# Kernel tuning notes

Hardware: AMD Instinct MI355X
Metric: run time of the kernel (lower is better)

The kernel has to match this reference:

```python
import jax, jax.numpy as jnp
import numpy as np

NUM_CONCEPTS = 4096
CONCEPT_DIM = 512


def setup_inputs() -> dict:
    key = jax.random.key(0)
    k1, k2 = jax.random.split(key)
    inp = jax.random.normal(k1, (8, 4096, CONCEPT_DIM), dtype=jnp.float32)
    bound = 1.0 / NUM_CONCEPTS
    codebook = jax.random.uniform(
        k2, (NUM_CONCEPTS, CONCEPT_DIM), dtype=jnp.float32,
        minval=-bound, maxval=bound)
    return {"inp": inp, "codebook": codebook}


def reference(inp, codebook):
    # flatten tokens: [N, D]
    flat = inp.reshape(-1, inp.shape[-1])
    # squared Euclidean distances [N, K]; argmin is identical to cdist argmin
    d2 = (
        jnp.sum(flat * flat, axis=1, keepdims=True)
        - 2.0 * jnp.einsum("nd,kd->nk", flat, codebook)
        + jnp.sum(codebook * codebook, axis=1)[None, :]
    )
    idx = jnp.argmin(d2, axis=1)  # [N]
    quantized = jnp.take(codebook, idx, axis=0).reshape(inp.shape)
    return quantized
```

## Files before the change

### kernel.cpp

```cpp
#include <hip/hip_runtime.h>
#include <math.h>

constexpr int D  = 512;
constexpr int K  = 4096;
constexpr int BM = 64;
constexpr int BN = 64;
constexpr int BD_LEG = 32;
constexpr int PAD = 4;

#define MARGIN 2.5e-3f
constexpr int RCAP = 12;
constexpr unsigned CAPQ = 4194304u;

typedef short short8v __attribute__((ext_vector_type(8)));
typedef float f32x4   __attribute__((ext_vector_type(4)));
typedef int   int4v   __attribute__((ext_vector_type(4)));

constexpr size_t SC_OFF   = 0;
constexpr size_t SX_OFF   = 16384;
constexpr size_t KEYS_OFF = 147456;
constexpr size_t QCNT_OFF = 409600;
constexpr size_t SCS_OFF  = 413696;
constexpr size_t SXS_OFF  = 430080;
constexpr size_t CBP_OFF  = 561152;
constexpr size_t WS_NEED  = CBP_OFF + (size_t)K * D;

__device__ inline unsigned ordkey(float f) {
    unsigned u = __float_as_uint(f);
    return (u & 0x80000000u) ? ~u : (u | 0x80000000u);
}
__device__ inline float fromkey(unsigned k) {
    unsigned u = (k & 0x80000000u) ? (k ^ 0x80000000u) : ~k;
    return __uint_as_float(u);
}
__device__ inline void gload16(const void* g, void* l) {
    __builtin_amdgcn_global_load_lds(
        (const __attribute__((address_space(1))) unsigned*)g,
        (__attribute__((address_space(3))) unsigned*)l, 16, 0, 0);
}

__global__ __launch_bounds__(256)
void prep_kernel(const float* __restrict__ cb, const float* __restrict__ inp,
                 float* __restrict__ sc, float* __restrict__ scs,
                 unsigned char* __restrict__ cbp,
                 float* __restrict__ sxg, float* __restrict__ sxs,
                 unsigned char* __restrict__ ap,
                 unsigned* __restrict__ qcnt, int nb_cb) {
    const int t = threadIdx.x;
    if (blockIdx.x == 0 && t == 0) *qcnt = 0u;
    const bool isCB = (int)blockIdx.x < nb_cb;
    const int r = t >> 2, p = t & 3;
    const int row = (isCB ? (int)blockIdx.x : ((int)blockIdx.x - nb_cb)) * 64 + r;
    const float* base = (isCB ? cb : inp) + (size_t)row * D + p * 128;

    float s = 0.0f, m = 0.0f;
#pragma unroll
    for (int g = 0; g < 16; ++g) {
        float4 v0 = *(const float4*)(base + g * 8);
        float4 v1 = *(const float4*)(base + g * 8 + 4);
        s = fmaf(v0.x, v0.x, s); s = fmaf(v0.y, v0.y, s);
        s = fmaf(v0.z, v0.z, s); s = fmaf(v0.w, v0.w, s);
        s = fmaf(v1.x, v1.x, s); s = fmaf(v1.y, v1.y, s);
        s = fmaf(v1.z, v1.z, s); s = fmaf(v1.w, v1.w, s);
        m = fmaxf(m, fmaxf(fmaxf(fabsf(v0.x), fabsf(v0.y)), fmaxf(fabsf(v0.z), fabsf(v0.w))));
        m = fmaxf(m, fmaxf(fmaxf(fabsf(v1.x), fabsf(v1.y)), fmaxf(fabsf(v1.z), fabsf(v1.w))));
    }
    s += __shfl_xor(s, 1, 64);
    s += __shfl_xor(s, 2, 64);
    m = fmaxf(m, __shfl_xor(m, 1, 64));
    m = fmaxf(m, __shfl_xor(m, 2, 64));
    const float sinv  = (m > 0.0f) ? 127.0f / m : 0.0f;
    const float scale = m * (1.0f / 127.0f);
    if (p == 0) {
        if (isCB) { sc[row] = s;  scs[row] = scale; }
        else      { sxg[row] = s; sxs[row] = scale; }
    }

    const int rstride = isCB ? 256 : 128;
    const int tile    = isCB ? (row >> 8) : (row >> 7);
    const int rit     = isCB ? (row & 255) : (row & 127);
    unsigned char* dst = isCB ? cbp : ap;
    const size_t tbase = (size_t)tile * (32 * rstride);
#pragma unroll
    for (int g = 0; g < 16; ++g) {
        float4 v0 = *(const float4*)(base + g * 8);
        float4 v1 = *(const float4*)(base + g * 8 + 4);
        float xs[8] = {v0.x, v0.y, v0.z, v0.w, v1.x, v1.y, v1.z, v1.w};
        unsigned u0 = 0, u1 = 0;
#pragma unroll
        for (int i = 0; i < 4; ++i) {
            int q = (int)rintf(xs[i] * sinv);
            q = q > 127 ? 127 : (q < -127 ? -127 : q);
            u0 |= ((unsigned)(q & 255)) << (8 * i);
        }
#pragma unroll
        for (int i = 4; i < 8; ++i) {
            int q = (int)rintf(xs[i] * sinv);
            q = q > 127 ? 127 : (q < -127 ? -127 : q);
            u1 |= ((unsigned)(q & 255)) << (8 * (i - 4));
        }
        const int db = 2 * p + (g >> 3);
        const int j  = ((16 * p + g) >> 1) & 3;
        const size_t slot = tbase + (size_t)db * (4 * rstride) + (size_t)j * rstride + rit;
        *(unsigned*)(dst + slot * 16 + (g & 1) * 8)     = u0;
        *(unsigned*)(dst + slot * 16 + (g & 1) * 8 + 4) = u1;
    }
}

__device__ float exact_dot512(const float* __restrict__ x, const float* __restrict__ c) {
    float s = 0.0f;
#pragma unroll 4
    for (int i = 0; i < 128; ++i) {
        const float4 xv = *(const float4*)(x + i * 4);
        const float4 cv = *(const float4*)(c + i * 4);
        s = fmaf(xv.x, cv.x, s); s = fmaf(xv.y, cv.y, s);
        s = fmaf(xv.z, cv.z, s); s = fmaf(xv.w, cv.w, s);
    }
    return s;
}

__global__ __launch_bounds__(512)
void score_kernel(const unsigned char* __restrict__ a_perm,
                  const unsigned char* __restrict__ b_perm,
                  const float* __restrict__ sc, const float* __restrict__ scs,
                  const float* __restrict__ sxs,
                  char* __restrict__ records) {
    __shared__ __align__(16) unsigned char lds[2 * 24576];
    __shared__ unsigned minsh[128];
    __shared__ unsigned cntsh[128];
    __shared__ unsigned short listsh[128][RCAP];

    const int t    = threadIdx.x;
    const int lane = t & 63;
    const int w    = t >> 6;
    const int wm   = w >> 2;
    const int wn   = w & 3;
    const int l15  = lane & 15;
    const int lk   = lane >> 4;
    const int bm   = blockIdx.x >> 4;
    const int bn   = blockIdx.x & 15;

    const unsigned char* gA = a_perm + (size_t)bm * 65536  + (size_t)t * 16;
    const unsigned char* gB = b_perm + (size_t)bn * 131072 + (size_t)t * 16;

    if (t < 128) { minsh[t] = 0xFFFFFFFFu; cntsh[t] = 0u; }

    int4v acc[4][4];
#pragma unroll
    for (int i = 0; i < 4; ++i)
#pragma unroll
        for (int j = 0; j < 4; ++j) acc[i][j] = int4v{0, 0, 0, 0};

    auto STAGE = [&](int db, int dbuf) {
        gload16(gA + (size_t)db * 8192,         &lds[dbuf + t * 16]);
        gload16(gB + (size_t)db * 16384,        &lds[dbuf + 8192 + t * 16]);
        gload16(gB + (size_t)db * 16384 + 8192, &lds[dbuf + 16384 + t * 16]);
    };

    STAGE(0, 0);
    __syncthreads();

    const unsigned char* lbA = &lds[lk * 2048 + l15 * 16];
    const unsigned char* lbB = &lds[8192 + lk * 4096 + l15 * 16];
    const int mbase = wm * 1024;
    const int nbase = wn * 1024;

    auto COMPUTE = [&](int cur) {
        int4v af[4], bf[4];
#pragma unroll
        for (int mt = 0; mt < 4; ++mt)
            af[mt] = *(const int4v*)(lbA + cur + mbase + mt * 256);
#pragma unroll
        for (int nt = 0; nt < 4; ++nt)
            bf[nt] = *(const int4v*)(lbB + cur + nbase + nt * 256);
#pragma unroll
        for (int mt = 0; mt < 4; ++mt)
#pragma unroll
            for (int nt = 0; nt < 4; ++nt)
                acc[mt][nt] = __builtin_amdgcn_mfma_i32_16x16x64_i8(af[mt], bf[nt], acc[mt][nt], 0, 0, 0);
    };

    int sdb = 1;
#pragma unroll 1
    for (int p = 0; p < 4; ++p) {
        STAGE(sdb, 24576); ++sdb;
        COMPUTE(0);
        __syncthreads();
        if (p < 3) { STAGE(sdb, 0); ++sdb; }
        COMPUTE(24576);
        __syncthreads();
    }

    float scvv[4], scsv[4];
#pragma unroll
    for (int nt = 0; nt < 4; ++nt) {
        const int code = bn * 256 + wn * 64 + nt * 16 + l15;
        scvv[nt] = sc[code];
        scsv[nt] = scs[code];
    }
    float sxsv[4][4];
#pragma unroll
    for (int mt = 0; mt < 4; ++mt)
#pragma unroll
        for (int rr = 0; rr < 4; ++rr)
            sxsv[mt][rr] = sxs[bm * 128 + wm * 64 + mt * 16 + lk * 4 + rr];

#pragma unroll
    for (int mt = 0; mt < 4; ++mt)
#pragma unroll
        for (int nt = 0; nt < 4; ++nt)
#pragma unroll
            for (int rr = 0; rr < 4; ++rr) {
                const float df = (float)acc[mt][nt][rr];
                const float vv = fmaf(-2.0f * sxsv[mt][rr] * scsv[nt], df, scvv[nt]);
                acc[mt][nt][rr] = __float_as_int(vv);
            }
#define VACC(mt, nt, rr) __int_as_float(acc[mt][nt][rr])

#pragma unroll
    for (int mt = 0; mt < 4; ++mt)
#pragma unroll
        for (int rr = 0; rr < 4; ++rr) {
            float m4 = fminf(fminf(VACC(mt, 0, rr), VACC(mt, 1, rr)),
                             fminf(VACC(mt, 2, rr), VACC(mt, 3, rr)));
            m4 = fminf(m4, __shfl_xor(m4, 1, 64));
            m4 = fminf(m4, __shfl_xor(m4, 2, 64));
            m4 = fminf(m4, __shfl_xor(m4, 4, 64));
            m4 = fminf(m4, __shfl_xor(m4, 8, 64));
            if (l15 == 0) {
                const int tok = wm * 64 + mt * 16 + lk * 4 + rr;
                atomicMin(&minsh[tok], ordkey(m4));
            }
        }
    __syncthreads();

#pragma unroll
    for (int mt = 0; mt < 4; ++mt)
#pragma unroll
        for (int rr = 0; rr < 4; ++rr) {
            const int tok = wm * 64 + mt * 16 + lk * 4 + rr;
            const float tmn = fromkey(minsh[tok]) + MARGIN;
#pragma unroll
            for (int nt = 0; nt < 4; ++nt) {
                if (VACC(mt, nt, rr) <= tmn) {
                    unsigned p = atomicAdd(&cntsh[tok], 1u);
                    if (p < RCAP)
                        listsh[tok][p] = (unsigned short)(bn * 256 + wn * 64 + nt * 16 + l15);
                }
            }
        }
    __syncthreads();
#undef VACC

    if (t < 128) {
        const unsigned* lw = (const unsigned*)&listsh[t][0];
        uint4 r0, r1;
        r0.x = __float_as_uint(fromkey(minsh[t]));
        r0.y = cntsh[t];
        r0.z = lw[0]; r0.w = lw[1];
        r1.x = lw[2]; r1.y = lw[3]; r1.z = lw[4]; r1.w = lw[5];
        char* rp = records + ((size_t)(bm * 128 + t) * 16 + bn) * 32;
        *(uint4*)rp = r0;
        *(uint4*)(rp + 16) = r1;
    }
}

__global__ __launch_bounds__(256)
void compact_kernel(const char* __restrict__ records,
                    unsigned long long* __restrict__ keysg,
                    unsigned* __restrict__ qcnt,
                    unsigned* __restrict__ queue) {
    const int token = blockIdx.x * 256 + threadIdx.x;
    keysg[token] = 0xFFFFFFFFFFFFFFFFull;

    const char* rbase = records + (size_t)token * 16 * 32;
    float mn = __builtin_huge_valf();
#pragma unroll
    for (int i = 0; i < 16; ++i)
        mn = fminf(mn, *(const float*)(rbase + (size_t)i * 32));
    const float thr = mn + MARGIN;

    unsigned my = 0;
#pragma unroll 1
    for (int i = 0; i < 16; ++i) {
        const char* rp = rbase + (size_t)i * 32;
        if (*(const float*)rp <= thr) {
            const unsigned cnt = *(const unsigned*)(rp + 4);
            my += (cnt <= RCAP) ? cnt : 256u;
        }
    }
    unsigned pos = atomicAdd(qcnt, my);
#pragma unroll 1
    for (int i = 0; i < 16; ++i) {
        const char* rp = rbase + (size_t)i * 32;
        if (*(const float*)rp <= thr) {
            const unsigned cnt = *(const unsigned*)(rp + 4);
            if (cnt <= RCAP) {
                const unsigned short* cs = (const unsigned short*)(rp + 8);
                for (unsigned j = 0; j < cnt; ++j) {
                    if (pos < CAPQ) queue[pos] = ((unsigned)token << 12) | cs[j];
                    ++pos;
                }
            } else {
                for (int c2 = 0; c2 < 256; ++c2) {
                    if (pos < CAPQ) queue[pos] = ((unsigned)token << 12) | (unsigned)(i * 256 + c2);
                    ++pos;
                }
            }
        }
    }
}

__global__ __launch_bounds__(256)
void exec_kernel(const float* __restrict__ inp, const float* __restrict__ cb,
                 const float* __restrict__ sc, const float* __restrict__ sxg,
                 const unsigned* __restrict__ qcnt, const unsigned* __restrict__ queue,
                 unsigned long long* __restrict__ keysg, int nblk64) {
    const unsigned raw = *qcnt;
    unsigned total = raw > CAPQ ? CAPQ : raw;
    const unsigned stride = gridDim.x * 256;
    for (unsigned i = blockIdx.x * 256 + threadIdx.x; i < total; i += stride) {
        const unsigned e = queue[i];
        const int token = e >> 12;
        const int code  = e & 4095;
        const float dot = exact_dot512(inp + (size_t)token * D, cb + (size_t)code * D);
        const float tmp = sxg[token] - 2.0f * dot;
        const float v   = tmp + sc[code];
        const unsigned long long key =
            ((unsigned long long)__float_as_uint(v) << 32) | (unsigned)code;
        atomicMin(&keysg[token], key);
    }
    if (raw > CAPQ && blockIdx.x < (unsigned)nblk64) {
        const int t = threadIdx.x;
        const int m0 = blockIdx.x * 64;
#pragma unroll 1
        for (int tok = 0; tok < 64; ++tok) {
            const int token = m0 + tok;
            const float sxv = sxg[token];
            const float* xrow = inp + (size_t)token * D;
            for (int code = t; code < K; code += 256) {
                const float dot = exact_dot512(xrow, cb + (size_t)code * D);
                const float tmp = sxv - 2.0f * dot;
                const float v   = tmp + sc[code];
                const unsigned long long key =
                    ((unsigned long long)__float_as_uint(v) << 32) | (unsigned)code;
                atomicMin(&keysg[token], key);
            }
        }
    }
}

__global__ __launch_bounds__(256)
void gather_kernel(const float* __restrict__ cb,
                   const unsigned long long* __restrict__ keysg,
                   float* __restrict__ out) {
    const int m0 = blockIdx.x * 64;
    __shared__ int bidx[64];
    if (threadIdx.x < 64) bidx[threadIdx.x] = (int)(keysg[m0 + threadIdx.x] & 0xFFFFFFFFull);
    __syncthreads();
    for (int q = threadIdx.x; q < 64 * (D / 4); q += 256) {
        const int r = q >> 7;
        const int c = (q & 127) * 4;
        *(float4*)(out + (size_t)(m0 + r) * D + c) = *(const float4*)(cb + (size_t)bidx[r] * D + c);
    }
}

__global__ __launch_bounds__(256)
void sc_kernel(const float* __restrict__ cb, float* __restrict__ sc) {
    const int row  = blockIdx.x * 4 + (threadIdx.x >> 6);
    const int lane = threadIdx.x & 63;
    const float* r = cb + (size_t)row * D + lane * 8;
    float4 v0 = *(const float4*)r;
    float4 v1 = *(const float4*)(r + 4);
    float s = v0.x * v0.x;
    s += v0.y * v0.y; s += v0.z * v0.z; s += v0.w * v0.w;
    s += v1.x * v1.x; s += v1.y * v1.y; s += v1.z * v1.z; s += v1.w * v1.w;
#pragma unroll
    for (int off = 1; off < 64; off <<= 1) s += __shfl_xor(s, off, 64);
    if (lane == 0) sc[row] = s;
}

__global__ __launch_bounds__(256)
void vq_kernel(const float* __restrict__ inp, const float* __restrict__ cb,
               const float* __restrict__ sc, float* __restrict__ out) {
    __shared__ __align__(16) float As[BD_LEG][BM + PAD];
    __shared__ __align__(16) float Bs[BD_LEG][BN + PAD];
    __shared__ float sxl[BM];
    __shared__ float scs_l[BN];
    __shared__ int   bidx[BM];

    const int t  = threadIdx.x;
    const int m0 = blockIdx.x * BM;
    const int tm = t >> 4;
    const int tn = t & 15;
    const float FINF = __builtin_huge_valf();

    {
        const int r = t >> 2, p = t & 3;
        const float* row = inp + (size_t)(m0 + r) * D + p * 128;
        float s = 0.0f;
#pragma unroll
        for (int i = 0; i < 32; ++i) {
            float4 v = *(const float4*)(row + i * 4);
            s = fmaf(v.x, v.x, s); s = fmaf(v.y, v.y, s);
            s = fmaf(v.z, v.z, s); s = fmaf(v.w, v.w, s);
        }
        s += __shfl_xor(s, 1, 64);
        s += __shfl_xor(s, 2, 64);
        if (p == 0) sxl[r] = s;
    }
    __syncthreads();

    float sxm[4];
#pragma unroll
    for (int i = 0; i < 4; ++i) sxm[i] = sxl[tm * 4 + i];

    float runv[4] = {FINF, FINF, FINF, FINF};
    int   runi[4] = {0, 0, 0, 0};
    const int dq = (t & 7) << 2;
    const int mr = t >> 3;

#pragma unroll 1
    for (int kb = 0; kb < K; kb += BN) {
        __syncthreads();
        if (t < BN) scs_l[t] = sc[kb + t];

        float accl[4][4];
#pragma unroll
        for (int i = 0; i < 4; ++i)
#pragma unroll
            for (int j = 0; j < 4; ++j) accl[i][j] = 0.0f;

#pragma unroll 1
        for (int db = 0; db < D; db += BD_LEG) {
            const float* ap = inp + (size_t)(m0 + mr) * D + db + dq;
            const float* bp = cb  + (size_t)(kb + mr) * D + db + dq;
            float4 av0 = *(const float4*)ap;
            float4 av1 = *(const float4*)(ap + (size_t)32 * D);
            float4 bv0 = *(const float4*)bp;
            float4 bv1 = *(const float4*)(bp + (size_t)32 * D);
            __syncthreads();
            As[dq + 0][mr] = av0.x; As[dq + 1][mr] = av0.y;
            As[dq + 2][mr] = av0.z; As[dq + 3][mr] = av0.w;
            As[dq + 0][mr + 32] = av1.x; As[dq + 1][mr + 32] = av1.y;
            As[dq + 2][mr + 32] = av1.z; As[dq + 3][mr + 32] = av1.w;
            Bs[dq + 0][mr] = bv0.x; Bs[dq + 1][mr] = bv0.y;
            Bs[dq + 2][mr] = bv0.z; Bs[dq + 3][mr] = bv0.w;
            Bs[dq + 0][mr + 32] = bv1.x; Bs[dq + 1][mr + 32] = bv1.y;
            Bs[dq + 2][mr + 32] = bv1.z; Bs[dq + 3][mr + 32] = bv1.w;
            __syncthreads();
#pragma unroll
            for (int d = 0; d < BD_LEG; ++d) {
                const float4 a = *(const float4*)(&As[d][tm * 4]);
                const float4 b = *(const float4*)(&Bs[d][tn * 4]);
                float af[4] = {a.x, a.y, a.z, a.w};
                float bf[4] = {b.x, b.y, b.z, b.w};
#pragma unroll
                for (int i = 0; i < 4; ++i)
#pragma unroll
                    for (int j = 0; j < 4; ++j)
                        accl[i][j] = fmaf(af[i], bf[j], accl[i][j]);
            }
        }
#pragma unroll
        for (int i = 0; i < 4; ++i) {
            float bv = FINF;
            int   bi = 0x7fffffff;
#pragma unroll
            for (int j = 0; j < 4; ++j) {
                const float p = accl[i][j];
                const float tmp = sxm[i] - 2.0f * p;
                const float v   = tmp + scs_l[tn * 4 + j];
                const int  idx  = kb + tn * 4 + j;
                if (v < bv) { bv = v; bi = idx; }
            }
#pragma unroll
            for (int off = 1; off < 16; off <<= 1) {
                const float ov = __shfl_xor(bv, off, 64);
                const int   oi = __shfl_xor(bi, off, 64);
                if (ov < bv || (ov == bv && oi < bi)) { bv = ov; bi = oi; }
            }
            if (bv < runv[i]) { runv[i] = bv; runi[i] = bi; }
        }
    }
    if (tn == 0) {
#pragma unroll
        for (int i = 0; i < 4; ++i) bidx[tm * 4 + i] = runi[i];
    }
    __syncthreads();
#pragma unroll 1
    for (int q = t; q < BM * (D / 4); q += 256) {
        const int r = q >> 7;
        const int c = (q & 127) * 4;
        const float4 v = *(const float4*)(cb + (size_t)bidx[r] * D + c);
        *(float4*)(out + (size_t)(m0 + r) * D + c) = v;
    }
}

extern "C" void kernel_launch(void* const* d_in, const int* in_sizes, int n_in,
                              void* d_out, int out_size, void* d_ws, size_t ws_size,
                              hipStream_t stream) {
    const float* inp = (const float*)d_in[0];
    const float* cb  = (const float*)d_in[1];
    float* out = (float*)d_out;
    float* sc  = (float*)d_ws;
    const int tokens = in_sizes[0] / D;

    const bool fast = (ws_size >= WS_NEED) && (tokens % 256 == 0) &&
                      (in_sizes[1] == K * D) &&
                      ((size_t)out_size * 4 >= (size_t)tokens * D + (size_t)tokens * 16 * 32);

    if (fast) {
        float* sxg = (float*)((char*)d_ws + SX_OFF);
        unsigned long long* keysg = (unsigned long long*)((char*)d_ws + KEYS_OFF);
        unsigned* qcnt = (unsigned*)((char*)d_ws + QCNT_OFF);
        float* scsg = (float*)((char*)d_ws + SCS_OFF);
        float* sxsg = (float*)((char*)d_ws + SXS_OFF);
        unsigned char* cbp = (unsigned char*)((char*)d_ws + CBP_OFF);
        unsigned char* ap  = (unsigned char*)d_out;
        char* records = (char*)d_out + (size_t)tokens * D;
        unsigned* queue = (unsigned*)d_out;

        const int nb_cb = K / 64;

        prep_kernel<<<nb_cb + tokens / 64, 256, 0, stream>>>(cb, inp, sc, scsg, cbp,
                                                             sxg, sxsg, ap, qcnt, nb_cb);
        score_kernel<<<(tokens / 128) * 16, 512, 0, stream>>>(ap, cbp, sc, scsg, sxsg, records);
        compact_kernel<<<tokens / 256, 256, 0, stream>>>(records, keysg, qcnt, queue);
        exec_kernel<<<2048, 256, 0, stream>>>(inp, cb, sc, sxg, qcnt, queue, keysg, tokens / 64);
        gather_kernel<<<tokens / 64, 256, 0, stream>>>(cb, keysg, out);
    } else {
        sc_kernel<<<K / 4, 256, 0, stream>>>(cb, sc);
        vq_kernel<<<tokens / BM, 256, 0, stream>>>(inp, cb, sc, out);
    }
}
```

Before: 286.9 us.

## Fuse compact, exec and gather into one per-block resolve kernel with LDS queue

Replaces the global candidate queue, global atomic counter and three separate kernels (compact, exact-rescore, gather) with a single resolve kernel in which each 64-token block builds its candidate list in shared memory, rescores candidates exactly with LDS atomicMin, and gathers the winning codebook rows. This removes two kernel launches, the global queue traffic and the global atomics. In exchange, parallelism is limited to tokens/64 blocks, so load imbalance between blocks is possible, and any block whose list overflows LCAP falls back to a full 4096-code brute-force scan done by that one block.

```diff
diff --git a/kernel.cpp b/kernel.cpp
--- a/kernel.cpp
+++ b/kernel.cpp
@@ -10,7 +10,7 @@
 
 #define MARGIN 2.5e-3f
 constexpr int RCAP = 12;
-constexpr unsigned CAPQ = 4194304u;
+constexpr int LCAP = 3072;
 
 typedef short short8v __attribute__((ext_vector_type(8)));
 typedef float f32x4   __attribute__((ext_vector_type(4)));
@@ -18,11 +18,9 @@
 
 constexpr size_t SC_OFF   = 0;
 constexpr size_t SX_OFF   = 16384;
-constexpr size_t KEYS_OFF = 147456;
-constexpr size_t QCNT_OFF = 409600;
-constexpr size_t SCS_OFF  = 413696;
-constexpr size_t SXS_OFF  = 430080;
-constexpr size_t CBP_OFF  = 561152;
+constexpr size_t SCS_OFF  = 147456;
+constexpr size_t SXS_OFF  = 163840;
+constexpr size_t CBP_OFF  = 294912;
 constexpr size_t WS_NEED  = CBP_OFF + (size_t)K * D;
 
 __device__ inline unsigned ordkey(float f) {
@@ -44,10 +42,8 @@
                  float* __restrict__ sc, float* __restrict__ scs,
                  unsigned char* __restrict__ cbp,
                  float* __restrict__ sxg, float* __restrict__ sxs,
-                 unsigned char* __restrict__ ap,
-                 unsigned* __restrict__ qcnt, int nb_cb) {
+                 unsigned char* __restrict__ ap, int nb_cb) {
     const int t = threadIdx.x;
-    if (blockIdx.x == 0 && t == 0) *qcnt = 0u;
     const bool isCB = (int)blockIdx.x < nb_cb;
     const int r = t >> 2, p = t & 3;
     const int row = (isCB ? (int)blockIdx.x : ((int)blockIdx.x - nb_cb)) * 64 + r;
@@ -266,99 +262,95 @@
 }
 
 __global__ __launch_bounds__(256)
-void compact_kernel(const char* __restrict__ records,
-                    unsigned long long* __restrict__ keysg,
-                    unsigned* __restrict__ qcnt,
-                    unsigned* __restrict__ queue) {
-    const int token = blockIdx.x * 256 + threadIdx.x;
-    keysg[token] = 0xFFFFFFFFFFFFFFFFull;
-
-    const char* rbase = records + (size_t)token * 16 * 32;
-    float mn = __builtin_huge_valf();
-#pragma unroll
-    for (int i = 0; i < 16; ++i)
-        mn = fminf(mn, *(const float*)(rbase + (size_t)i * 32));
-    const float thr = mn + MARGIN;
-
-    unsigned my = 0;
-#pragma unroll 1
-    for (int i = 0; i < 16; ++i) {
-        const char* rp = rbase + (size_t)i * 32;
-        if (*(const float*)rp <= thr) {
-            const unsigned cnt = *(const unsigned*)(rp + 4);
-            my += (cnt <= RCAP) ? cnt : 256u;
-        }
-    }
-    unsigned pos = atomicAdd(qcnt, my);
-#pragma unroll 1
-    for (int i = 0; i < 16; ++i) {
-        const char* rp = rbase + (size_t)i * 32;
-        if (*(const float*)rp <= thr) {
-            const unsigned cnt = *(const unsigned*)(rp + 4);
-            if (cnt <= RCAP) {
-                const unsigned short* cs = (const unsigned short*)(rp + 8);
-                for (unsigned j = 0; j < cnt; ++j) {
-                    if (pos < CAPQ) queue[pos] = ((unsigned)token << 12) | cs[j];
-                    ++pos;
+void resolve_kernel(const float* __restrict__ inp, const float* __restrict__ cb,
+                    const float* __restrict__ sc, const float* __restrict__ sxg,
+                    const char* __restrict__ records, float* __restrict__ out) {
+    __shared__ unsigned long long keysh[64];
+    __shared__ unsigned qtot;
+    __shared__ unsigned listq[LCAP];
+    __shared__ int bidx[64];
+
+    const int t  = threadIdx.x;
+    const int m0 = blockIdx.x * 64;
+
+    if (t < 64) keysh[t] = 0xFFFFFFFFFFFFFFFFull;
+    if (t == 0) qtot = 0u;
+    __syncthreads();
+
+    if (t < 64) {
+        const char* rbase = records + (size_t)(m0 + t) * 16 * 32;
+        float mn = __builtin_huge_valf();
+#pragma unroll
+        for (int i = 0; i < 16; ++i)
+            mn = fminf(mn, *(const float*)(rbase + (size_t)i * 32));
+        const float thr = mn + MARGIN;
+
+        unsigned my = 0;
+#pragma unroll 1
+        for (int i = 0; i < 16; ++i) {
+            const char* rp = rbase + (size_t)i * 32;
+            if (*(const float*)rp <= thr) {
+                const unsigned cnt = *(const unsigned*)(rp + 4);
+                my += (cnt <= RCAP) ? cnt : 256u;
+            }
+        }
+        unsigned pos = atomicAdd(&qtot, my);
+#pragma unroll 1
+        for (int i = 0; i < 16; ++i) {
+            const char* rp = rbase + (size_t)i * 32;
+            if (*(const float*)rp <= thr) {
+                const unsigned cnt = *(const unsigned*)(rp + 4);
+                if (cnt <= RCAP) {
+                    const unsigned short* cs = (const unsigned short*)(rp + 8);
+                    for (unsigned j = 0; j < cnt; ++j) {
+                        if (pos < LCAP) listq[pos] = ((unsigned)t << 12) | cs[j];
+                        ++pos;
+                    }
+                } else {
+                    for (int c2 = 0; c2 < 256; ++c2) {
+                        if (pos < LCAP) listq[pos] = ((unsigned)t << 12) | (unsigned)(i * 256 + c2);
+                        ++pos;
+                    }
                 }
-            } else {
-                for (int c2 = 0; c2 < 256; ++c2) {
-                    if (pos < CAPQ) queue[pos] = ((unsigned)token << 12) | (unsigned)(i * 256 + c2);
-                    ++pos;
-                }
-            }
-        }
-    }
-}
-
-__global__ __launch_bounds__(256)
-void exec_kernel(const float* __restrict__ inp, const float* __restrict__ cb,
-                 const float* __restrict__ sc, const float* __restrict__ sxg,
-                 const unsigned* __restrict__ qcnt, const unsigned* __restrict__ queue,
-                 unsigned long long* __restrict__ keysg, int nblk64) {
-    const unsigned raw = *qcnt;
-    unsigned total = raw > CAPQ ? CAPQ : raw;
-    const unsigned stride = gridDim.x * 256;
-    for (unsigned i = blockIdx.x * 256 + threadIdx.x; i < total; i += stride) {
-        const unsigned e = queue[i];
-        const int token = e >> 12;
-        const int code  = e & 4095;
-        const float dot = exact_dot512(inp + (size_t)token * D, cb + (size_t)code * D);
-        const float tmp = sxg[token] - 2.0f * dot;
-        const float v   = tmp + sc[code];
-        const unsigned long long key =
-            ((unsigned long long)__float_as_uint(v) << 32) | (unsigned)code;
-        atomicMin(&keysg[token], key);
-    }
-    if (raw > CAPQ && blockIdx.x < (unsigned)nblk64) {
-        const int t = threadIdx.x;
-        const int m0 = blockIdx.x * 64;
+            }
+        }
+    }
+    __syncthreads();
+
+    const unsigned total = qtot;
+    if (total <= (unsigned)LCAP) {
+        for (unsigned i = t; i < total; i += 256) {
+            const unsigned e = listq[i];
+            const int tok  = e >> 12;
+            const int code = e & 4095;
+            const float dot = exact_dot512(inp + (size_t)(m0 + tok) * D, cb + (size_t)code * D);
+            const float tmp = sxg[m0 + tok] - 2.0f * dot;
+            const float v   = tmp + sc[code];
+            const unsigned long long key =
+                ((unsigned long long)__float_as_uint(v) << 32) | (unsigned)code;
+            atomicMin(&keysh[tok], key);
+        }
+    } else {
 #pragma unroll 1
         for (int tok = 0; tok < 64; ++tok) {
-            const int token = m0 + tok;
-            const float sxv = sxg[token];
-            const float* xrow = inp + (size_t)token * D;
+            const float sxv = sxg[m0 + tok];
+            const float* xrow = inp + (size_t)(m0 + tok) * D;
             for (int code = t; code < K; code += 256) {
                 const float dot = exact_dot512(xrow, cb + (size_t)code * D);
                 const float tmp = sxv - 2.0f * dot;
                 const float v   = tmp + sc[code];
                 const unsigned long long key =
                     ((unsigned long long)__float_as_uint(v) << 32) | (unsigned)code;
-                atomicMin(&keysg[token], key);
-            }
-        }
-    }
-}
-
-__global__ __launch_bounds__(256)
-void gather_kernel(const float* __restrict__ cb,
-                   const unsigned long long* __restrict__ keysg,
-                   float* __restrict__ out) {
-    const int m0 = blockIdx.x * 64;
-    __shared__ int bidx[64];
-    if (threadIdx.x < 64) bidx[threadIdx.x] = (int)(keysg[m0 + threadIdx.x] & 0xFFFFFFFFull);
-    __syncthreads();
-    for (int q = threadIdx.x; q < 64 * (D / 4); q += 256) {
+                atomicMin(&keysh[tok], key);
+            }
+        }
+    }
+    __syncthreads();
+
+    if (t < 64) bidx[t] = (int)(keysh[t] & 0xFFFFFFFFull);
+    __syncthreads();
+
+    for (int q = t; q < 64 * (D / 4); q += 256) {
         const int r = q >> 7;
         const int c = (q & 127) * 4;
         *(float4*)(out + (size_t)(m0 + r) * D + c) = *(const float4*)(cb + (size_t)bidx[r] * D + c);
@@ -512,23 +504,18 @@
 
     if (fast) {
         float* sxg = (float*)((char*)d_ws + SX_OFF);
-        unsigned long long* keysg = (unsigned long long*)((char*)d_ws + KEYS_OFF);
-        unsigned* qcnt = (unsigned*)((char*)d_ws + QCNT_OFF);
         float* scsg = (float*)((char*)d_ws + SCS_OFF);
         float* sxsg = (float*)((char*)d_ws + SXS_OFF);
         unsigned char* cbp = (unsigned char*)((char*)d_ws + CBP_OFF);
         unsigned char* ap  = (unsigned char*)d_out;
         char* records = (char*)d_out + (size_t)tokens * D;
-        unsigned* queue = (unsigned*)d_out;
 
         const int nb_cb = K / 64;
 
         prep_kernel<<<nb_cb + tokens / 64, 256, 0, stream>>>(cb, inp, sc, scsg, cbp,
-                                                             sxg, sxsg, ap, qcnt, nb_cb);
+                                                             sxg, sxsg, ap, nb_cb);
         score_kernel<<<(tokens / 128) * 16, 512, 0, stream>>>(ap, cbp, sc, scsg, sxsg, records);
-        compact_kernel<<<tokens / 256, 256, 0, stream>>>(records, keysg, qcnt, queue);
-        exec_kernel<<<2048, 256, 0, stream>>>(inp, cb, sc, sxg, qcnt, queue, keysg, tokens / 64);
-        gather_kernel<<<tokens / 64, 256, 0, stream>>>(cb, keysg, out);
+        resolve_kernel<<<tokens / 64, 256, 0, stream>>>(inp, cb, sc, sxg, records, out);
     } else {
         sc_kernel<<<K / 4, 256, 0, stream>>>(cb, sc);
         vq_kernel<<<tokens / BM, 256, 0, stream>>>(inp, cb, sc, out);
```

Result: faster. 262.6 us, median of 2 (-8.5%).
